# Kernel tuning notes

Hardware: AMD Instinct MI355X
Metric: run time of the kernel (lower is better)

## Reference

```python
import jax, jax.numpy as jnp
import numpy as np

NUM_HEADS = 8
BLOCK_SIZE = 32   # tokens per block
WINDOW = 64       # window radius in blocks -> attends to blocks [i-64, i+64]


def setup_inputs() -> dict:
    key = jax.random.key(0)
    ks = jax.random.split(key, 5)
    B, N, C = 8, 8192, 512
    s = 0.02
    return {
        "x": jax.random.normal(ks[0], (B, N, C), dtype=jnp.float32),
        # torch Linear(dim, 3*dim): y = x @ W.T + b; we store W already transposed [in, out]
        "W_qkv": jax.random.normal(ks[1], (C, 3 * C), dtype=jnp.float32) * s,
        "b_qkv": jax.random.normal(ks[2], (3 * C,), dtype=jnp.float32) * s,
        "W_proj": jax.random.normal(ks[3], (C, C), dtype=jnp.float32) * s,
        "b_proj": jax.random.normal(ks[4], (C,), dtype=jnp.float32) * s,
    }


def reference(x, W_qkv, b_qkv, W_proj, b_proj):
    B, N, C = x.shape
    h = NUM_HEADS
    dh = C // h
    scale = jnp.asarray(dh, x.dtype) ** -0.5

    # qkv projection, then the module's head-interleaved split:
    # rearrange 'b n (h d) -> b h n d' with d = 3C/h, chunk(3) on last dim,
    # rearrange back 'b h n d -> b n (h d)'. Equivalent to:
    qkv = (x @ W_qkv + b_qkv).reshape(B, N, h, 3 * dh)
    q = qkv[..., :dh].reshape(B, N, C)
    k = qkv[..., dh:2 * dh].reshape(B, N, C)
    v = qkv[..., 2 * dh:].reshape(B, N, C)

    # dynamic blocking (N chosen divisible by BLOCK_SIZE -> no padding)
    nb = N // BLOCK_SIZE
    qb = q.reshape(B, nb, BLOCK_SIZE, C)
    kb = k.reshape(B, nb, BLOCK_SIZE, C)
    vb = v.reshape(B, nb, BLOCK_SIZE, C)

    # per-offset block attention: query block i, position s attends to
    # position s of every block j in [i-WINDOW, i+WINDOW]
    attn = jnp.einsum('bisc,bjsc->bisj', qb, kb) * scale  # [B, nb, s, nb]
    i_idx = jnp.arange(nb)[:, None]
    j_idx = jnp.arange(nb)[None, :]
    band = (j_idx >= i_idx - WINDOW) & (j_idx <= i_idx + WINDOW)  # [nb, nb]
    neg = jnp.finfo(attn.dtype).min
    attn = jnp.where(band[None, :, None, :], attn, neg)
    attn = jax.nn.softmax(attn, axis=-1)
    out = jnp.einsum('bisj,bjsc->bisc', attn, vb)  # [B, nb, s, C]
    out = out.reshape(B, N, C)

    # 'b n (h d) -> b n h d -> b n (h d)' is the identity
    return out @ W_proj + b_proj
```

## Files before the change

kernel.cpp:

```cpp
#include <hip/hip_runtime.h>
#include <hip/hip_bf16.h>
#include <stdint.h>

#define B_   8
#define N_   8192
#define C_   512
#define NB   256
#define WIN  64

typedef __attribute__((ext_vector_type(8))) short short8;
typedef __attribute__((ext_vector_type(4))) float f32x4;
typedef __hip_bfloat16 bf16;

__device__ __forceinline__ void gload_lds16(const void* g, void* l) {
  __builtin_amdgcn_global_load_lds((const __attribute__((address_space(1))) void*)g,
                                   (__attribute__((address_space(3))) void*)l, 16, 0, 0);
}

__device__ __forceinline__ f32x4 mfma16(short8 a, short8 b, f32x4 c) {
  return __builtin_amdgcn_mfma_f32_16x16x32_bf16(a, b, c, 0, 0, 0);
}


__global__ __launch_bounds__(256) void k_conv_x(const float4* __restrict__ x,
                                                ushort4* __restrict__ xb) {
  size_t idx = (size_t)blockIdx.x * 256 + threadIdx.x;
  float4 v = x[idx];
  union { ushort4 u; bf16 b[4]; } o;
  o.b[0] = __float2bfloat16(v.x); o.b[1] = __float2bfloat16(v.y);
  o.b[2] = __float2bfloat16(v.z); o.b[3] = __float2bfloat16(v.w);
  xb[idx] = o.u;
}

__global__ __launch_bounds__(256) void k_conv_w(const float* __restrict__ W,
                                                const float* __restrict__ bsrc,
                                                bf16* __restrict__ Wt,
                                                float* __restrict__ bperm,
                                                int ldw, int qkv) {
  __shared__ float tile[32][65];
  const int cc = blockIdx.x, k0 = blockIdx.y * 32;
  const int src0 = cc * 64;
  const int o0 = qkv ? ((cc % 3) * 512 + (cc / 3) * 64) : src0;
  const int tid = threadIdx.x;
#pragma unroll
  for (int q = 0; q < 8; ++q) {
    int li = q * 256 + tid;
    int r = li >> 6, c = li & 63;
    tile[r][c] = W[(size_t)(k0 + r) * ldw + src0 + c];
  }
  __syncthreads();
#pragma unroll
  for (int q = 0; q < 8; ++q) {
    int li = q * 256 + tid;
    int c2 = li >> 5, kk = li & 31;
    Wt[(size_t)(o0 + c2) * 512 + k0 + kk] = __float2bfloat16(tile[kk][c2]);
  }
  if (qkv && blockIdx.y == 0 && tid < 64) bperm[o0 + tid] = bsrc[src0 + tid];
}

template <int EPI>
__global__ __launch_bounds__(512, 2) void k_gemm(const bf16* __restrict__ A,
                                                 const bf16* __restrict__ Bt,
                                                 const float* __restrict__ bias,
                                                 bf16* __restrict__ qb,
                                                 bf16* __restrict__ kb,
                                                 bf16* __restrict__ vb,
                                                 float* __restrict__ outf,
                                                 int NT) {
  extern __shared__ char gsm[];
  const int tid = threadIdx.x;
  const int lane = tid & 63, wid = tid >> 6;
  const int wr = wid >> 2, wcn = wid & 3;
  const int l15 = lane & 15, l4 = lane >> 4;

  const int nwg = gridDim.x;
  const int cpx = nwg >> 3;
  const int swz = (blockIdx.x & 7) * cpx + (blockIdx.x >> 3);
  const int mt = swz / NT, nt = swz % NT;
  const size_t m0 = (size_t)mt * 256;
  const int n0 = nt * 256;

  f32x4 acc[8][4];
#pragma unroll
  for (int fi = 0; fi < 8; ++fi)
#pragma unroll
    for (int fj = 0; fj < 4; ++fj) acc[fi][fj] = (f32x4){0.f, 0.f, 0.f, 0.f};

#define STAGE(K0)                                                              \
  {                                                                            \
    _Pragma("unroll") for (int q = 0; q < 4; ++q) {                            \
      int li = q * 512 + tid;                                                  \
      int r = li >> 3, g = (li & 7) ^ (r & 7);                                 \
      gload_lds16(A + (m0 + r) * 512 + (K0) + g * 8, gsm + li * 16);           \
    }                                                                          \
    _Pragma("unroll") for (int q = 0; q < 4; ++q) {                            \
      int li = q * 512 + tid;                                                  \
      int r = li >> 3, g = (li & 7) ^ (r & 7);                                 \
      gload_lds16(Bt + (size_t)(n0 + r) * 512 + (K0) + g * 8,                  \
                  gsm + 32768 + li * 16);                                      \
    }                                                                          \
  }

  STAGE(0);
  for (int t = 0; t < 8; ++t) {
    asm volatile("s_waitcnt vmcnt(0)" ::: "memory");
    __builtin_amdgcn_s_barrier();
    __builtin_amdgcn_sched_barrier(0);
    const char* Ab = gsm;
    const char* Bb = gsm + 32768;

    short8 bf2[4][2], a0f[4][2], a1f[4][2];
#pragma unroll
    for (int f = 0; f < 4; ++f) {
      int rb = f * 64 + wcn * 16 + l15;
      const char* base = Bb + rb * 128;
      bf2[f][0] = *(const short8*)(base + ((l4 ^ (rb & 7)) << 4));
      bf2[f][1] = *(const short8*)(base + (((4 + l4) ^ (rb & 7)) << 4));
    }
#pragma unroll
    for (int f = 0; f < 4; ++f) {
      int ra = f * 32 + wr * 16 + l15;
      const char* base = Ab + ra * 128;
      a0f[f][0] = *(const short8*)(base + ((l4 ^ (ra & 7)) << 4));
      a0f[f][1] = *(const short8*)(base + (((4 + l4) ^ (ra & 7)) << 4));
    }
    __builtin_amdgcn_s_setprio(1);
#pragma unroll
    for (int f = 0; f < 4; ++f)
#pragma unroll
      for (int g = 0; g < 4; ++g) {
        acc[f][g] = mfma16(a0f[f][0], bf2[g][0], acc[f][g]);
        acc[f][g] = mfma16(a0f[f][1], bf2[g][1], acc[f][g]);
      }
    __builtin_amdgcn_s_setprio(0);
#pragma unroll
    for (int f = 0; f < 4; ++f) {
      int ra = 128 + f * 32 + wr * 16 + l15;
      const char* base = Ab + ra * 128;
      a1f[f][0] = *(const short8*)(base + ((l4 ^ (ra & 7)) << 4));
      a1f[f][1] = *(const short8*)(base + (((4 + l4) ^ (ra & 7)) << 4));
    }
    __builtin_amdgcn_s_setprio(1);
#pragma unroll
    for (int f = 0; f < 4; ++f)
#pragma unroll
      for (int g = 0; g < 4; ++g) {
        acc[4 + f][g] = mfma16(a1f[f][0], bf2[g][0], acc[4 + f][g]);
        acc[4 + f][g] = mfma16(a1f[f][1], bf2[g][1], acc[4 + f][g]);
      }
    __builtin_amdgcn_s_setprio(0);

    __builtin_amdgcn_sched_barrier(0);
    asm volatile("s_waitcnt lgkmcnt(0)" ::: "memory");
    __builtin_amdgcn_s_barrier();
    __builtin_amdgcn_sched_barrier(0);
    if (t < 7) STAGE((t + 1) * 64);
  }
#undef STAGE

  if (EPI == 0) {
#pragma unroll
    for (int fi = 0; fi < 8; ++fi)
#pragma unroll
      for (int fj = 0; fj < 4; ++fj) {
        int o = n0 + fj * 64 + wcn * 16 + l15;
        float bia = bias[o];
        int part = o >> 9;
        int c = o & 511;
        bf16* dst = part == 0 ? qb : (part == 1 ? kb : vb);
#pragma unroll
        for (int r = 0; r < 4; ++r) {
          size_t m = m0 + fi * 32 + wr * 16 + l4 * 4 + r;
          int bidx = (int)(m >> 13);
          int n = (int)(m & 8191);
          int blk = n >> 5, s = n & 31;
          size_t di = (((size_t)(bidx * 32 + s) * 256 + blk) << 9) | c;
          dst[di] = __float2bfloat16(acc[fi][fj][r] + bia);
        }
      }
  } else {
#pragma unroll
    for (int fi = 0; fi < 8; ++fi)
#pragma unroll
      for (int fj = 0; fj < 4; ++fj) {
        int o = n0 + fj * 64 + wcn * 16 + l15;
        float bia = bias[o];
#pragma unroll
        for (int r = 0; r < 4; ++r) {
          size_t m = m0 + fi * 32 + wr * 16 + l4 * 4 + r;
          outf[m * 512 + o] = acc[fi][fj][r] + bia;
        }
      }
  }
}

__global__ __launch_bounds__(256) void k_transpose_v(const bf16* __restrict__ v,
                                                     bf16* __restrict__ vT) {
  __shared__ bf16 t[32][36];
  int bs = blockIdx.x, j0 = blockIdx.y * 32, c0 = blockIdx.z * 32;
  const bf16* src = v + (size_t)bs * NB * C_;
  bf16* dst = vT + (size_t)bs * C_ * NB;
  int r = threadIdx.x >> 3, c4 = (threadIdx.x & 7) * 4;
  *(ushort4*)&t[r][c4] = *(const ushort4*)(src + (size_t)(j0 + r) * C_ + c0 + c4);
  __syncthreads();
  union { ushort4 u; bf16 b[4]; } o;
  o.b[0] = t[c4 + 0][r]; o.b[1] = t[c4 + 1][r];
  o.b[2] = t[c4 + 2][r]; o.b[3] = t[c4 + 3][r];
  *(ushort4*)(dst + (size_t)(c0 + r) * NB + j0 + c4) = o.u;
}

#define QS_OFF   0
#define KB_OFF   32768
#define VB_OFF   98304
#define SS_OFF   131072
#define PS_OFF   135296
#define SR_OFF   137856
#define MR_OFF   141952
#define LR_OFF   142080
#define AL_OFF   142208
#define ATTN_LDS 142336

__global__ __launch_bounds__(512) void k_attn(const bf16* __restrict__ qg,
                                              const bf16* __restrict__ kg,
                                              const bf16* __restrict__ vTg,
                                              bf16* __restrict__ outb) {
  extern __shared__ char smc[];
  float* Ssf  = (float*)(smc + SS_OFF);
  bf16*  Psb  = (bf16*)(smc + PS_OFF);
  float* Sred = (float*)(smc + SR_OFF);
  float* mrow = (float*)(smc + MR_OFF);
  float* lrow = (float*)(smc + LR_OFF);
  float* alph = (float*)(smc + AL_OFF);

  const int tid = threadIdx.x, lane = tid & 63, wid = tid >> 6;
  const int l15 = lane & 15, l4 = lane >> 4;
  const int gt = (blockIdx.x & 7) * 256 + (blockIdx.x >> 3);
  const int bs = gt >> 3;
  const int b = bs >> 5, s = bs & 31;
  const int i0 = (gt & 7) * 32;
  const int jlo = max(0, i0 - WIN);
  const int jhi = min(NB - 1, i0 + 31 + WIN);
  const int nch = (jhi - jlo + 1) >> 5;
  const bf16* Qb = qg + (size_t)bs * NB * C_;
  const bf16* Kb = kg + (size_t)bs * NB * C_;
  const bf16* Vb = vTg + (size_t)bs * C_ * NB;

  const int qh_qk = (wid >> 2) & 1, jh = (wid >> 1) & 1, ks = wid & 1;
  const int qh_pv = wid >> 2, cq = wid & 3;

  f32x4 O[8];
#pragma unroll
  for (int f = 0; f < 8; ++f) O[f] = (f32x4){0.f, 0.f, 0.f, 0.f};

  if (tid < 32) { mrow[tid] = -1e30f; lrow[tid] = 0.f; }

#pragma unroll
  for (int q = 0; q < 4; ++q) {
    int li = q * 512 + tid;
    int row = li >> 6, g = (li & 63) ^ (row & 15);
    gload_lds16(Qb + (size_t)(i0 + row) * C_ + g * 8, smc + QS_OFF + li * 16);
  }
#pragma unroll
  for (int q = 0; q < 4; ++q) {
    int li = q * 512 + tid;
    int row = li >> 6, g = (li & 63) ^ (row & 15);
    gload_lds16(Kb + (size_t)(jlo + row) * C_ + g * 8, smc + KB_OFF + li * 16);
  }

  for (int t = 0; t < nch; ++t) {
    const int j0 = jlo + t * 32;
    asm volatile("s_waitcnt vmcnt(0) lgkmcnt(0)" ::: "memory");
    __builtin_amdgcn_s_barrier();
    __builtin_amdgcn_sched_barrier(0);

#pragma unroll
    for (int q = 0; q < 4; ++q) {
      int li = q * 512 + tid;
      int c = li >> 2, g = (li & 3) ^ (c & 3);
      gload_lds16(Vb + (size_t)c * NB + j0 + g * 8, smc + VB_OFF + li * 16);
    }
    if (t + 1 < nch) {
      int jn = j0 + 32;
      char* kdst = smc + KB_OFF + ((t + 1) & 1) * 32768;
#pragma unroll
      for (int q = 0; q < 4; ++q) {
        int li = q * 512 + tid;
        int row = li >> 6, g = (li & 63) ^ (row & 15);
        gload_lds16(Kb + (size_t)(jn + row) * C_ + g * 8, kdst + li * 16);
      }
    }

    {
      const int arow = qh_qk * 16 + l15;
      const int brow = jh * 16 + l15;
      const char* Qbase = smc + QS_OFF + arow * 1024;
      const char* Kbase = smc + KB_OFF + (t & 1) * 32768 + brow * 1024;
      f32x4 a0 = (f32x4){0.f, 0.f, 0.f, 0.f}, a1 = a0;
      __builtin_amdgcn_s_setprio(1);
#pragma unroll
      for (int cc = 0; cc < 8; ++cc) {
        int sa = (ks * 32 + cc * 4 + l4) ^ (arow & 15);
        int sb = (ks * 32 + cc * 4 + l4) ^ (brow & 15);
        short8 av = *(const short8*)(Qbase + sa * 16);
        short8 bv = *(const short8*)(Kbase + sb * 16);
        if (cc & 1) a1 = mfma16(av, bv, a1);
        else        a0 = mfma16(av, bv, a0);
      }
      __builtin_amdgcn_s_setprio(0);
      f32x4 acc = a0 + a1;
      if (ks) {
        *(f32x4*)&Sred[(wid >> 1) * 256 + lane * 4] = acc;
      }
      asm volatile("s_waitcnt lgkmcnt(0)" ::: "memory");
      __builtin_amdgcn_s_barrier();
      __builtin_amdgcn_sched_barrier(0);
      if (!ks) {
        f32x4 su = acc + *(f32x4*)&Sred[(wid >> 1) * 256 + lane * 4];
        int jg = j0 + jh * 16 + l15;
#pragma unroll
        for (int r = 0; r < 4; ++r) {
          int i_in = qh_qk * 16 + l4 * 4 + r;
          int i_abs = i0 + i_in;
          bool valid = (jg >= i_abs - WIN) && (jg <= i_abs + WIN);
          Ssf[i_in * 33 + jh * 16 + l15] = valid ? su[r] * 0.125f : -1e30f;
        }
      }
      asm volatile("s_waitcnt lgkmcnt(0)" ::: "memory");
      __builtin_amdgcn_s_barrier();
      __builtin_amdgcn_sched_barrier(0);
    }

    {
      int row = tid >> 4, u = tid & 15;
      float s0 = Ssf[row * 33 + u], s1 = Ssf[row * 33 + u + 16];
      float mc = fmaxf(s0, s1);
      mc = fmaxf(mc, __shfl_xor(mc, 1));
      mc = fmaxf(mc, __shfl_xor(mc, 2));
      mc = fmaxf(mc, __shfl_xor(mc, 4));
      mc = fmaxf(mc, __shfl_xor(mc, 8));
      float mo = mrow[row];
      float mn = fmaxf(mo, mc);
      float a = __expf(mo - mn);
      float p0 = __expf(s0 - mn), p1 = __expf(s1 - mn);
      float ps = p0 + p1;
      ps += __shfl_xor(ps, 1);
      ps += __shfl_xor(ps, 2);
      ps += __shfl_xor(ps, 4);
      ps += __shfl_xor(ps, 8);
      if (u == 0) {
        lrow[row] = lrow[row] * a + ps;
        mrow[row] = mn;
        alph[row] = a;
      }
      Psb[row * 40 + u] = __float2bfloat16(p0);
      Psb[row * 40 + u + 16] = __float2bfloat16(p1);
    }
    if (t + 1 < nch)
      asm volatile("s_waitcnt vmcnt(4) lgkmcnt(0)" ::: "memory");
    else
      asm volatile("s_waitcnt vmcnt(0) lgkmcnt(0)" ::: "memory");
    __builtin_amdgcn_s_barrier();
    __builtin_amdgcn_sched_barrier(0);

    {
      float ar[4];
#pragma unroll
      for (int r = 0; r < 4; ++r) ar[r] = alph[qh_pv * 16 + l4 * 4 + r];
      short8 pa = *(const short8*)(smc + PS_OFF + (qh_pv * 16 + l15) * 80 + l4 * 16);
      __builtin_amdgcn_s_setprio(1);
#pragma unroll
      for (int f = 0; f < 8; ++f) {
        int c = cq * 128 + f * 16 + l15;
        short8 vv = *(const short8*)(smc + VB_OFF + c * 64 + ((l4 ^ (c & 3)) << 4));
#pragma unroll
        for (int r = 0; r < 4; ++r) O[f][r] *= ar[r];
        O[f] = mfma16(pa, vv, O[f]);
      }
      __builtin_amdgcn_s_setprio(0);
    }
    __builtin_amdgcn_sched_barrier(0);
  }

  asm volatile("s_waitcnt lgkmcnt(0)" ::: "memory");
  __builtin_amdgcn_s_barrier();
  {
    float lr[4];
#pragma unroll
    for (int r = 0; r < 4; ++r) lr[r] = 1.f / lrow[qh_pv * 16 + l4 * 4 + r];
#pragma unroll
    for (int f = 0; f < 8; ++f) {
      int c = cq * 128 + f * 16 + l15;
#pragma unroll
      for (int r = 0; r < 4; ++r) {
        int il = qh_pv * 16 + l4 * 4 + r;
        int n = (i0 + il) * 32 + s;
        outb[((size_t)b * N_ + n) * C_ + c] = __float2bfloat16(O[f][r] * lr[r]);
      }
    }
  }
}

extern "C" void kernel_launch(void* const* d_in, const int* in_sizes, int n_in,
                              void* d_out, int out_size, void* d_ws, size_t ws_size,
                              hipStream_t stream) {
  const float* x = (const float*)d_in[0];
  const float* Wqkv = (const float*)d_in[1];
  const float* bqkv = (const float*)d_in[2];
  const float* Wproj = (const float*)d_in[3];
  const float* bproj = (const float*)d_in[4];

  char* ws = (char*)d_ws;
  const size_t SLOT = 67108864ull;
  bf16* slotA = (bf16*)ws;
  bf16* slotB = (bf16*)(ws + SLOT);
  bf16* Wqkv_t = (bf16*)(ws + 2 * SLOT);
  bf16* Wproj_t = (bf16*)(ws + 2 * SLOT + 1572864);
  float* bias_perm = (float*)(ws + 2 * SLOT + 1572864 + 524288);
  bf16* qbuf = (bf16*)d_out;
  bf16* kbuf = qbuf + 33554432ull;

  static int attr_done = 0;
  if (!attr_done) {
    hipFuncSetAttribute((const void*)k_gemm<0>,
                        hipFuncAttributeMaxDynamicSharedMemorySize, 65536);
    hipFuncSetAttribute((const void*)k_gemm<1>,
                        hipFuncAttributeMaxDynamicSharedMemorySize, 65536);
    hipFuncSetAttribute((const void*)k_attn,
                        hipFuncAttributeMaxDynamicSharedMemorySize, ATTN_LDS);
    attr_done = 1;
  }

  k_conv_x<<<32768, 256, 0, stream>>>((const float4*)x, (ushort4*)slotA);
  k_conv_w<<<dim3(24, 16), 256, 0, stream>>>(Wqkv, bqkv, Wqkv_t, bias_perm, 1536, 1);
  k_conv_w<<<dim3(8, 16), 256, 0, stream>>>(Wproj, nullptr, Wproj_t, nullptr, 512, 0);

  k_gemm<0><<<1536, 512, 65536, stream>>>(slotA, Wqkv_t, bias_perm,
                                          qbuf, kbuf, slotB, nullptr, 6);
  k_transpose_v<<<dim3(256, 8, 16), 256, 0, stream>>>(slotB, slotA);
  k_attn<<<2048, 512, ATTN_LDS, stream>>>(qbuf, kbuf, slotA, slotB);
  k_gemm<1><<<512, 512, 65536, stream>>>(slotB, Wproj_t, bproj,
                                         nullptr, nullptr, nullptr, (float*)d_out, 2);
}
```

Before: 351.7 us.

## Fuse x fp32-to-bf16 conversion into QKV GEMM and double-buffer GEMM LDS

Removes the separate x conversion kernel; the QKV GEMM now loads fp32 x into registers, converts to bf16 and writes swizzled LDS itself. Both GEMMs switch to double-buffered LDS (128KB), prefetching the next K-slice while computing the current one. This cuts a full read/write pass over the activation, at the cost of rereading fp32 x per N-tile and reduced occupancy from doubled LDS.

```diff
diff --git a/kernel.cpp b/kernel.cpp
--- a/kernel.cpp
+++ b/kernel.cpp
@@ -19,17 +19,6 @@
 
 __device__ __forceinline__ f32x4 mfma16(short8 a, short8 b, f32x4 c) {
   return __builtin_amdgcn_mfma_f32_16x16x32_bf16(a, b, c, 0, 0, 0);
-}
-
-
-__global__ __launch_bounds__(256) void k_conv_x(const float4* __restrict__ x,
-                                                ushort4* __restrict__ xb) {
-  size_t idx = (size_t)blockIdx.x * 256 + threadIdx.x;
-  float4 v = x[idx];
-  union { ushort4 u; bf16 b[4]; } o;
-  o.b[0] = __float2bfloat16(v.x); o.b[1] = __float2bfloat16(v.y);
-  o.b[2] = __float2bfloat16(v.z); o.b[3] = __float2bfloat16(v.w);
-  xb[idx] = o.u;
 }
 
 __global__ __launch_bounds__(256) void k_conv_w(const float* __restrict__ W,
@@ -58,13 +47,159 @@
   if (qkv && blockIdx.y == 0 && tid < 64) bperm[o0 + tid] = bsrc[src0 + tid];
 }
 
-template <int EPI>
+__global__ __launch_bounds__(512, 2) void k_gemm_x(const float* __restrict__ X,
+                                                   const bf16* __restrict__ Bt,
+                                                   const float* __restrict__ bias,
+                                                   bf16* __restrict__ qb,
+                                                   bf16* __restrict__ kb,
+                                                   bf16* __restrict__ vb,
+                                                   int NT) {
+  extern __shared__ char gsm[];
+  const int tid = threadIdx.x;
+  const int lane = tid & 63, wid = tid >> 6;
+  const int wr = wid >> 2, wcn = wid & 3;
+  const int l15 = lane & 15, l4 = lane >> 4;
+
+  const int nwg = gridDim.x;
+  const int cpx = nwg >> 3;
+  const int swz = (blockIdx.x & 7) * cpx + (blockIdx.x >> 3);
+  const int mt = swz / NT, nt = swz % NT;
+  const size_t m0 = (size_t)mt * 256;
+  const int n0 = nt * 256;
+
+  f32x4 acc[8][4];
+#pragma unroll
+  for (int fi = 0; fi < 8; ++fi)
+#pragma unroll
+    for (int fj = 0; fj < 4; ++fj) acc[fi][fj] = (f32x4){0.f, 0.f, 0.f, 0.f};
+
+  float4 va[4][2];
+
+#define ISSUE_A(K0)                                                            \
+  { _Pragma("unroll") for (int q2 = 0; q2 < 4; ++q2) {                         \
+      int G = q2 * 512 + tid;                                                  \
+      int r = G >> 3, g = G & 7;                                               \
+      const float* p = X + (m0 + r) * 512 + (K0) + g * 8;                      \
+      va[q2][0] = *(const float4*)p;                                           \
+      va[q2][1] = *(const float4*)(p + 4);                                     \
+    } }
+#define WRITE_A(E)                                                             \
+  { _Pragma("unroll") for (int q2 = 0; q2 < 4; ++q2) {                         \
+      int G = q2 * 512 + tid;                                                  \
+      int r = G >> 3, g = G & 7, slot = g ^ (r & 7);                           \
+      union { bf16 b[8]; short8 s; } pk;                                       \
+      _Pragma("unroll") for (int j = 0; j < 4; ++j) {                          \
+        pk.b[j] = __float2bfloat16(va[q2][0][j]);                              \
+        pk.b[4 + j] = __float2bfloat16(va[q2][1][j]);                          \
+      }                                                                        \
+      *(short8*)(gsm + (E) * 65536 + (r * 8 + slot) * 16) = pk.s;              \
+    } }
+#define ISSUE_B(E, K0)                                                         \
+  { _Pragma("unroll") for (int q = 0; q < 4; ++q) {                            \
+      int li = q * 512 + tid;                                                  \
+      int r = li >> 3, g = (li & 7) ^ (r & 7);                                 \
+      gload_lds16(Bt + (size_t)(n0 + r) * 512 + (K0) + g * 8,                  \
+                  gsm + (E) * 65536 + 32768 + li * 16);                        \
+    } }
+
+  ISSUE_A(0);
+  __builtin_amdgcn_sched_barrier(0);
+  ISSUE_B(0, 0);
+  __builtin_amdgcn_sched_barrier(0);
+  WRITE_A(0);
+  asm volatile("s_waitcnt vmcnt(0)" ::: "memory");
+  asm volatile("s_waitcnt lgkmcnt(0)" ::: "memory");
+  __builtin_amdgcn_s_barrier();
+
+  for (int t = 0; t < 8; ++t) {
+    const int cur = t & 1, nxt = cur ^ 1;
+    if (t < 7) {
+      ISSUE_A((t + 1) * 64);
+      __builtin_amdgcn_sched_barrier(0);
+      ISSUE_B(nxt, (t + 1) * 64);
+      __builtin_amdgcn_sched_barrier(0);
+    }
+    const char* Ab = gsm + cur * 65536;
+    const char* Bb = Ab + 32768;
+
+    short8 bf2[4][2], a0f[4][2], a1f[4][2];
+#pragma unroll
+    for (int f = 0; f < 4; ++f) {
+      int rb = f * 64 + wcn * 16 + l15;
+      const char* base = Bb + rb * 128;
+      bf2[f][0] = *(const short8*)(base + ((l4 ^ (rb & 7)) << 4));
+      bf2[f][1] = *(const short8*)(base + (((4 + l4) ^ (rb & 7)) << 4));
+    }
+#pragma unroll
+    for (int f = 0; f < 4; ++f) {
+      int ra = f * 32 + wr * 16 + l15;
+      const char* base = Ab + ra * 128;
+      a0f[f][0] = *(const short8*)(base + ((l4 ^ (ra & 7)) << 4));
+      a0f[f][1] = *(const short8*)(base + (((4 + l4) ^ (ra & 7)) << 4));
+    }
+    __builtin_amdgcn_s_setprio(1);
+#pragma unroll
+    for (int f = 0; f < 4; ++f)
+#pragma unroll
+      for (int g = 0; g < 4; ++g) {
+        acc[f][g] = mfma16(a0f[f][0], bf2[g][0], acc[f][g]);
+        acc[f][g] = mfma16(a0f[f][1], bf2[g][1], acc[f][g]);
+      }
+    __builtin_amdgcn_s_setprio(0);
+#pragma unroll
+    for (int f = 0; f < 4; ++f) {
+      int ra = 128 + f * 32 + wr * 16 + l15;
+      const char* base = Ab + ra * 128;
+      a1f[f][0] = *(const short8*)(base + ((l4 ^ (ra & 7)) << 4));
+      a1f[f][1] = *(const short8*)(base + (((4 + l4) ^ (ra & 7)) << 4));
+    }
+    __builtin_amdgcn_s_setprio(1);
+#pragma unroll
+    for (int f = 0; f < 4; ++f)
+#pragma unroll
+      for (int g = 0; g < 4; ++g) {
+        acc[4 + f][g] = mfma16(a1f[f][0], bf2[g][0], acc[4 + f][g]);
+        acc[4 + f][g] = mfma16(a1f[f][1], bf2[g][1], acc[4 + f][g]);
+      }
+    __builtin_amdgcn_s_setprio(0);
+
+    if (t < 7) {
+      __builtin_amdgcn_sched_barrier(0);
+      WRITE_A(nxt);
+      asm volatile("s_waitcnt vmcnt(0)" ::: "memory");
+      asm volatile("s_waitcnt lgkmcnt(0)" ::: "memory");
+      __builtin_amdgcn_s_barrier();
+      __builtin_amdgcn_sched_barrier(0);
+    }
+  }
+#undef ISSUE_A
+#undef WRITE_A
+#undef ISSUE_B
+
+#pragma unroll
+  for (int fi = 0; fi < 8; ++fi)
+#pragma unroll
+    for (int fj = 0; fj < 4; ++fj) {
+      int o = n0 + fj * 64 + wcn * 16 + l15;
+      float bia = bias[o];
+      int part = o >> 9;
+      int c = o & 511;
+      bf16* dst = part == 0 ? qb : (part == 1 ? kb : vb);
+#pragma unroll
+      for (int r = 0; r < 4; ++r) {
+        size_t m = m0 + fi * 32 + wr * 16 + l4 * 4 + r;
+        int bidx = (int)(m >> 13);
+        int n = (int)(m & 8191);
+        int blk = n >> 5, s = n & 31;
+        size_t di = (((size_t)(bidx * 32 + s) * 256 + blk) << 9) | c;
+        dst[di] = __float2bfloat16(acc[fi][fj][r] + bia);
+      }
+    }
+}
+
 __global__ __launch_bounds__(512, 2) void k_gemm(const bf16* __restrict__ A,
                                                  const bf16* __restrict__ Bt,
                                                  const float* __restrict__ bias,
-                                                 bf16* __restrict__ qb,
-                                                 bf16* __restrict__ kb,
-                                                 bf16* __restrict__ vb,
                                                  float* __restrict__ outf,
                                                  int NT) {
   extern __shared__ char gsm[];
@@ -86,28 +221,34 @@
 #pragma unroll
     for (int fj = 0; fj < 4; ++fj) acc[fi][fj] = (f32x4){0.f, 0.f, 0.f, 0.f};
 
-#define STAGE(K0)                                                              \
+#define STAGE(E, K0)                                                           \
   {                                                                            \
     _Pragma("unroll") for (int q = 0; q < 4; ++q) {                            \
       int li = q * 512 + tid;                                                  \
       int r = li >> 3, g = (li & 7) ^ (r & 7);                                 \
-      gload_lds16(A + (m0 + r) * 512 + (K0) + g * 8, gsm + li * 16);           \
+      gload_lds16(A + (m0 + r) * 512 + (K0) + g * 8,                           \
+                  gsm + (E) * 65536 + li * 16);                                \
     }                                                                          \
     _Pragma("unroll") for (int q = 0; q < 4; ++q) {                            \
       int li = q * 512 + tid;                                                  \
       int r = li >> 3, g = (li & 7) ^ (r & 7);                                 \
       gload_lds16(Bt + (size_t)(n0 + r) * 512 + (K0) + g * 8,                  \
-                  gsm + 32768 + li * 16);                                      \
+                  gsm + (E) * 65536 + 32768 + li * 16);                        \
     }                                                                          \
   }
 
-  STAGE(0);
+  STAGE(0, 0);
+  asm volatile("s_waitcnt vmcnt(0)" ::: "memory");
+  __builtin_amdgcn_s_barrier();
+
   for (int t = 0; t < 8; ++t) {
-    asm volatile("s_waitcnt vmcnt(0)" ::: "memory");
-    __builtin_amdgcn_s_barrier();
-    __builtin_amdgcn_sched_barrier(0);
-    const char* Ab = gsm;
-    const char* Bb = gsm + 32768;
+    const int cur = t & 1, nxt = cur ^ 1;
+    if (t < 7) {
+      STAGE(nxt, (t + 1) * 64);
+      __builtin_amdgcn_sched_barrier(0);
+    }
+    const char* Ab = gsm + cur * 65536;
+    const char* Bb = Ab + 32768;
 
     short8 bf2[4][2], a0f[4][2], a1f[4][2];
 #pragma unroll
@@ -150,48 +291,28 @@
       }
     __builtin_amdgcn_s_setprio(0);
 
-    __builtin_amdgcn_sched_barrier(0);
-    asm volatile("s_waitcnt lgkmcnt(0)" ::: "memory");
-    __builtin_amdgcn_s_barrier();
-    __builtin_amdgcn_sched_barrier(0);
-    if (t < 7) STAGE((t + 1) * 64);
+    if (t < 7) {
+      __builtin_amdgcn_sched_barrier(0);
+      asm volatile("s_waitcnt vmcnt(0)" ::: "memory");
+      asm volatile("s_waitcnt lgkmcnt(0)" ::: "memory");
+      __builtin_amdgcn_s_barrier();
+      __builtin_amdgcn_sched_barrier(0);
+    }
   }
 #undef STAGE
 
-  if (EPI == 0) {
-#pragma unroll
-    for (int fi = 0; fi < 8; ++fi)
-#pragma unroll
-      for (int fj = 0; fj < 4; ++fj) {
-        int o = n0 + fj * 64 + wcn * 16 + l15;
-        float bia = bias[o];
-        int part = o >> 9;
-        int c = o & 511;
-        bf16* dst = part == 0 ? qb : (part == 1 ? kb : vb);
-#pragma unroll
-        for (int r = 0; r < 4; ++r) {
-          size_t m = m0 + fi * 32 + wr * 16 + l4 * 4 + r;
-          int bidx = (int)(m >> 13);
-          int n = (int)(m & 8191);
-          int blk = n >> 5, s = n & 31;
-          size_t di = (((size_t)(bidx * 32 + s) * 256 + blk) << 9) | c;
-          dst[di] = __float2bfloat16(acc[fi][fj][r] + bia);
-        }
-      }
-  } else {
-#pragma unroll
-    for (int fi = 0; fi < 8; ++fi)
-#pragma unroll
-      for (int fj = 0; fj < 4; ++fj) {
-        int o = n0 + fj * 64 + wcn * 16 + l15;
-        float bia = bias[o];
-#pragma unroll
-        for (int r = 0; r < 4; ++r) {
-          size_t m = m0 + fi * 32 + wr * 16 + l4 * 4 + r;
-          outf[m * 512 + o] = acc[fi][fj][r] + bia;
-        }
-      }
-  }
+#pragma unroll
+  for (int fi = 0; fi < 8; ++fi)
+#pragma unroll
+    for (int fj = 0; fj < 4; ++fj) {
+      int o = n0 + fj * 64 + wcn * 16 + l15;
+      float bia = bias[o];
+#pragma unroll
+      for (int r = 0; r < 4; ++r) {
+        size_t m = m0 + fi * 32 + wr * 16 + l4 * 4 + r;
+        outf[m * 512 + o] = acc[fi][fj][r] + bia;
+      }
+    }
 }
 
 __global__ __launch_bounds__(256) void k_transpose_v(const bf16* __restrict__ v,
@@ -421,23 +542,21 @@
 
   static int attr_done = 0;
   if (!attr_done) {
-    hipFuncSetAttribute((const void*)k_gemm<0>,
-                        hipFuncAttributeMaxDynamicSharedMemorySize, 65536);
-    hipFuncSetAttribute((const void*)k_gemm<1>,
-                        hipFuncAttributeMaxDynamicSharedMemorySize, 65536);
+    hipFuncSetAttribute((const void*)k_gemm_x,
+                        hipFuncAttributeMaxDynamicSharedMemorySize, 131072);
+    hipFuncSetAttribute((const void*)k_gemm,
+                        hipFuncAttributeMaxDynamicSharedMemorySize, 131072);
     hipFuncSetAttribute((const void*)k_attn,
                         hipFuncAttributeMaxDynamicSharedMemorySize, ATTN_LDS);
     attr_done = 1;
   }
 
-  k_conv_x<<<32768, 256, 0, stream>>>((const float4*)x, (ushort4*)slotA);
   k_conv_w<<<dim3(24, 16), 256, 0, stream>>>(Wqkv, bqkv, Wqkv_t, bias_perm, 1536, 1);
   k_conv_w<<<dim3(8, 16), 256, 0, stream>>>(Wproj, nullptr, Wproj_t, nullptr, 512, 0);
 
-  k_gemm<0><<<1536, 512, 65536, stream>>>(slotA, Wqkv_t, bias_perm,
-                                          qbuf, kbuf, slotB, nullptr, 6);
+  k_gemm_x<<<1536, 512, 131072, stream>>>(x, Wqkv_t, bias_perm,
+                                          qbuf, kbuf, slotB, 6);
   k_transpose_v<<<dim3(256, 8, 16), 256, 0, stream>>>(slotB, slotA);
   k_attn<<<2048, 512, ATTN_LDS, stream>>>(qbuf, kbuf, slotA, slotB);
-  k_gemm<1><<<512, 512, 65536, stream>>>(slotB, Wproj_t, bproj,
-                                         nullptr, nullptr, nullptr, (float*)d_out, 2);
-}
+  k_gemm<<<512, 512, 131072, stream>>>(slotB, Wproj_t, bproj, (float*)d_out, 2);
+}
```

New measurement: 367.6 us. 1.05x slower.
